# Kernel optimization log

Measured on AMD Instinct MI355X. Metric: run time of the kernel, lower is better.

The kernel has to match this reference:

```python
import jax, jax.numpy as jnp
import numpy as np

N = 50000      # nodes
E = 800000     # edges (avg degree 16)
F = 128        # num_features
H = 64         # nhid
S = 3          # num_scatter


def setup_inputs() -> dict:
    key = jax.random.key(0)
    ks = jax.random.split(key, 10)
    x = jax.random.normal(ks[0], (N, F), dtype=jnp.float32)
    scatter_edge_index = jax.random.randint(ks[1], (2, E), 0, N, dtype=jnp.int32)
    scatter_edge_attr = jax.random.normal(ks[2], (E,), dtype=jnp.float32)
    s = 0.05
    lin_W = jax.random.normal(ks[3], (F, H), dtype=jnp.float32) * s
    lin_b = jnp.zeros((H,), dtype=jnp.float32)
    # per-scatter-block 2-layer MLP applied after edge aggregation (layer=2)
    W1 = jax.random.normal(ks[4], (S, H, H), dtype=jnp.float32) * s
    b1 = jnp.zeros((S, H), dtype=jnp.float32)
    W2 = jax.random.normal(ks[5], (S, H, H), dtype=jnp.float32) * s
    b2 = jnp.zeros((S, H), dtype=jnp.float32)
    return {
        'x': x,
        'scatter_edge_index': scatter_edge_index,
        'scatter_edge_attr': scatter_edge_attr,
        'lin_W': lin_W, 'lin_b': lin_b,
        'W1': W1, 'b1': b1, 'W2': W2, 'b2': b2,
    }


def reference(x, scatter_edge_index, scatter_edge_attr, lin_W, lin_b, W1, b1, W2, b2):
    src = scatter_edge_index[0]
    dst = scatter_edge_index[1]
    attr = scatter_edge_attr[:, None]  # [E,1]

    def conv(h, i):
        # gather -> edge-weight -> scatter-add (message passing), then 2-layer MLP
        m = jax.ops.segment_sum(h[src] * attr, dst, num_segments=N)  # [N,H]
        t = jax.nn.relu(m @ W1[i] + b1[i])
        return t @ W2[i] + b2[i]

    h = x @ lin_W + lin_b  # lin_in (dropout is identity at eval)
    outs, scats = [], []
    for i in range(S):
        h = h + conv(h, i)          # residual accumulation
        outs.append(h)
        scats.append(conv(h, i))    # second conv on updated hidden_rep
    return (jnp.stack(scats), jnp.stack(outs))  # ([S,N,H], [S,N,H])
```

## Files before the change

### kernel.cpp

```cpp
#include <hip/hip_runtime.h>

#define NN 50000
#define NE 800000
#define FIN 128
#define HD 64
#define SL 3
#define GBM 782
#define NBIN 196
#define BSH 8

typedef __attribute__((ext_vector_type(8))) short bf16x8;
typedef __attribute__((ext_vector_type(4))) float f32x4;
#define MFMA(A, B, C) __builtin_amdgcn_mfma_f32_16x16x32_bf16(A, B, C, 0, 0, 0)


__device__ __forceinline__ unsigned int bfr(float x) {
    unsigned int u = __float_as_uint(x);
    return (u + 0x7fffu + ((u >> 16) & 1u)) >> 16;
}
__device__ __forceinline__ unsigned int bf2(float lo, float hi) {
    return bfr(lo) | (bfr(hi) << 16);
}


__global__ __launch_bounds__(256) void binhist_k(const int* __restrict__ dst,
                                                 int* __restrict__ bincnt) {
    __shared__ int h[256];
    int t = threadIdx.x;
    h[t] = 0;
    __syncthreads();
    int base = blockIdx.x * 4096;
    for (int i = t; i < 4096; i += 256) {
        int e = base + i;
        if (e < NE) atomicAdd(&h[dst[e] >> BSH], 1);
    }
    __syncthreads();
    if (t < NBIN && h[t]) atomicAdd(&bincnt[t], h[t]);
}

__global__ __launch_bounds__(256) void binscan_k(const int* __restrict__ bincnt,
                                                 int* __restrict__ binoff,
                                                 int* __restrict__ gbcur,
                                                 int* __restrict__ off) {
    __shared__ int sh[256];
    int t = threadIdx.x;
    int v = (t < NBIN) ? bincnt[t] : 0;
    sh[t] = v;
    __syncthreads();
    for (int d = 1; d < 256; d <<= 1) {
        int u = (t >= d) ? sh[t - d] : 0;
        __syncthreads();
        sh[t] += u;
        __syncthreads();
    }
    if (t < NBIN) {
        int ex = sh[t] - v;
        binoff[t] = ex;
        gbcur[t] = ex;
    }
    if (t == 255) {
        binoff[NBIN] = sh[255];
        off[NN] = sh[255];
    }
}

__global__ __launch_bounds__(256) void binpass_k(const int* __restrict__ src,
                                                 const int* __restrict__ dst,
                                                 const float* __restrict__ attr,
                                                 int* __restrict__ gbcur,
                                                 int2* __restrict__ tedge) {
    __shared__ int cnt_lds[256], runbase[256], lcur[256];
    int t = threadIdx.x;
    cnt_lds[t] = 0;
    lcur[t] = 0;
    __syncthreads();
    int base = blockIdx.x * 4096;
    for (int i = t; i < 4096; i += 256) {
        int e = base + i;
        if (e < NE) atomicAdd(&cnt_lds[dst[e] >> BSH], 1);
    }
    __syncthreads();
    if (t < NBIN && cnt_lds[t]) runbase[t] = atomicAdd(&gbcur[t], cnt_lds[t]);
    __syncthreads();
    for (int i = t; i < 4096; i += 256) {
        int e = base + i;
        if (e < NE) {
            int d = dst[e];
            int b = d >> BSH;
            int r = atomicAdd(&lcur[b], 1);
            tedge[runbase[b] + r] =
                make_int2(src[e] | ((d & 255) << 16), __float_as_int(attr[e]));
        }
    }
}

__global__ __launch_bounds__(256) void sortbin2_k(const int* __restrict__ binoff,
                                                  const int2* __restrict__ tedge,
                                                  int2* __restrict__ cedge,
                                                  int* __restrict__ off) {
    __shared__ int cnt[256], lofs[256], lcur[256];
    int b = blockIdx.x, t = threadIdx.x;
    int s = binoff[b], e = binoff[b + 1];
    cnt[t] = 0;
    __syncthreads();
    for (int i = s + t; i < e; i += 256)
        atomicAdd(&cnt[((unsigned)tedge[i].x >> 16) & 255], 1);
    __syncthreads();
    int v = cnt[t];
    lofs[t] = v;
    __syncthreads();
    for (int d = 1; d < 256; d <<= 1) {
        int u = (t >= d) ? lofs[t - d] : 0;
        __syncthreads();
        lofs[t] += u;
        __syncthreads();
    }
    int ex = lofs[t] - v;
    int node = (b << BSH) + t;
    if (node < NN) off[node] = s + ex;
    lcur[t] = ex;
    __syncthreads();
    for (int i = s + t; i < e; i += 256) {
        int2 ed = tedge[i];
        int dl = ((unsigned)ed.x >> 16) & 255;
        int p = s + atomicAdd(&lcur[dl], 1);
        cedge[p] = make_int2(ed.x & 0xffff, ed.y);
    }
}


__global__ __launch_bounds__(256) void wprep_k(const float* __restrict__ W1,
                                               const float* __restrict__ W2,
                                               const float* __restrict__ linW,
                                               short* __restrict__ prep) {
    int i = blockIdx.x * 256 + threadIdx.x;
    if (i < 24576) {
        int mat = i >> 12;
        int o = i & 4095;
        int j = o & 7, l = (o >> 3) & 63, s = (o >> 9) & 1, t = o >> 10;
        int k = 32 * s + 8 * (l >> 4) + j;
        int n = 16 * t + (l & 15);
        const float* Wsrc = (mat & 1) ? W2 : W1;
        prep[i] = (short)bfr(Wsrc[(mat >> 1) * 4096 + k * 64 + n]);
    } else if (i < 32768) {
        int o = i - 24576;
        int j = o & 7, l = (o >> 3) & 63, s = (o >> 9) & 3, t = o >> 11;
        int k = 32 * s + 8 * (l >> 4) + j;
        int n = 16 * t + (l & 15);
        prep[i] = (short)bfr(linW[k * 64 + n]);
    }
}


__global__ __launch_bounds__(256) void scatter_k(const uint4* __restrict__ hb4,
                                                 const int* __restrict__ off,
                                                 const int2* __restrict__ cedge,
                                                 uint4* __restrict__ mb4) {
    int w    = (blockIdx.x * blockDim.x + threadIdx.x) >> 6;
    int lane = threadIdx.x & 63;
    if (w >= NN) return;
    int g = lane >> 3;
    int f = lane & 7;
    int s = off[w], e = off[w + 1];
    float a0 = 0.f, a1 = 0.f, a2 = 0.f, a3 = 0.f;
    float a4 = 0.f, a5 = 0.f, a6 = 0.f, a7 = 0.f;
    for (int i = s + g; i < e; i += 8) {
        int2 ed = cedge[i];
        uint4 hv = hb4[(size_t)ed.x * 8 + f];
        float a = __int_as_float(ed.y);
        a0 += a * __uint_as_float(hv.x << 16);
        a1 += a * __uint_as_float(hv.x & 0xffff0000u);
        a2 += a * __uint_as_float(hv.y << 16);
        a3 += a * __uint_as_float(hv.y & 0xffff0000u);
        a4 += a * __uint_as_float(hv.z << 16);
        a5 += a * __uint_as_float(hv.z & 0xffff0000u);
        a6 += a * __uint_as_float(hv.w << 16);
        a7 += a * __uint_as_float(hv.w & 0xffff0000u);
    }
#pragma unroll
    for (int msk = 8; msk <= 32; msk <<= 1) {
        a0 += __shfl_xor(a0, msk);
        a1 += __shfl_xor(a1, msk);
        a2 += __shfl_xor(a2, msk);
        a3 += __shfl_xor(a3, msk);
        a4 += __shfl_xor(a4, msk);
        a5 += __shfl_xor(a5, msk);
        a6 += __shfl_xor(a6, msk);
        a7 += __shfl_xor(a7, msk);
    }
    if (g == 0) {
        uint4 o;
        o.x = bf2(a0, a1);
        o.y = bf2(a2, a3);
        o.z = bf2(a4, a5);
        o.w = bf2(a6, a7);
        mb4[(size_t)w * 8 + f] = o;
    }
}


__device__ __forceinline__ void conv_core(bf16x8 a0, bf16x8 a1,
                                          const bf16x8* __restrict__ w1f,
                                          const float* __restrict__ b1,
                                          const bf16x8* __restrict__ w2f,
                                          short* tw, int c, int q, int l,
                                          f32x4 oc[4]) {
    f32x4 acc[4];
#pragma unroll
    for (int t = 0; t < 4; t++) acc[t] = (f32x4){0.f, 0.f, 0.f, 0.f};
#pragma unroll
    for (int t = 0; t < 4; t++) {
        acc[t] = MFMA(a0, w1f[(t * 2 + 0) * 64 + l], acc[t]);
        acc[t] = MFMA(a1, w1f[(t * 2 + 1) * 64 + l], acc[t]);
    }
#pragma unroll
    for (int t = 0; t < 4; t++) {
        float bb = b1[16 * t + c];
#pragma unroll
        for (int rg = 0; rg < 4; rg++) {
            float v = fmaxf(acc[t][rg] + bb, 0.f);
            tw[(4 * q + rg) * 72 + 16 * t + c] = (short)bfr(v);
        }
    }
    __syncthreads();
    bf16x8 ta0 = *(const bf16x8*)&tw[c * 72 + 8 * q];
    bf16x8 ta1 = *(const bf16x8*)&tw[c * 72 + 32 + 8 * q];
#pragma unroll
    for (int t = 0; t < 4; t++) oc[t] = (f32x4){0.f, 0.f, 0.f, 0.f};
#pragma unroll
    for (int t = 0; t < 4; t++) {
        oc[t] = MFMA(ta0, w2f[(t * 2 + 0) * 64 + l], oc[t]);
        oc[t] = MFMA(ta1, w2f[(t * 2 + 1) * 64 + l], oc[t]);
    }
}


template <bool ADD, bool WB>
__global__ __launch_bounds__(256) void convm_k(const unsigned int* __restrict__ mb,
                                               const short* __restrict__ w1p,
                                               const float* __restrict__ b1,
                                               const short* __restrict__ w2p,
                                               const float* __restrict__ b2,
                                               const float* __restrict__ hprev,
                                               float* __restrict__ out,
                                               unsigned int* __restrict__ hb) {
    __shared__ short tls[4][16 * 72];
    int wv = threadIdx.x >> 6, l = threadIdx.x & 63;
    int c = l & 15, q = l >> 4;
    int rbase = blockIdx.x * 64 + wv * 16;

    int ar = rbase + c;
    bool aok = ar < NN;
    uint4 v0 = make_uint4(0, 0, 0, 0), v1 = v0;
    if (aok) {
        const uint4* mp = (const uint4*)(mb + (size_t)ar * 32);
        v0 = mp[q];
        v1 = mp[4 + q];
    }
    bf16x8 a0 = *(bf16x8*)&v0, a1 = *(bf16x8*)&v1;

    f32x4 oc[4];
    conv_core(a0, a1, (const bf16x8*)w1p, b1, (const bf16x8*)w2p, tls[wv], c, q, l, oc);

#pragma unroll
    for (int t = 0; t < 4; t++) {
        float bb = b2[16 * t + c];
#pragma unroll
        for (int rg = 0; rg < 4; rg++) {
            int row = rbase + 4 * q + rg;
            if (row < NN) {
                float v = oc[t][rg] + bb;
                if constexpr (ADD) v += hprev[(size_t)row * 64 + 16 * t + c];
                out[(size_t)row * 64 + 16 * t + c] = v;
                if constexpr (WB) {
                    float o = __shfl_xor(v, 1);
                    if ((c & 1) == 0)
                        hb[(size_t)row * 32 + 8 * t + (c >> 1)] = bf2(v, o);
                }
            }
        }
    }
}


__global__ __launch_bounds__(256) void conv2_k(const unsigned int* __restrict__ mb,
                                               const short* __restrict__ wa1,
                                               const float* __restrict__ ba1,
                                               const short* __restrict__ wa2,
                                               const float* __restrict__ ba2,
                                               const short* __restrict__ wb1,
                                               const float* __restrict__ bb1,
                                               const short* __restrict__ wb2,
                                               const float* __restrict__ bb2,
                                               const float* __restrict__ hprev,
                                               float* __restrict__ outa,
                                               float* __restrict__ outb,
                                               unsigned int* __restrict__ hb) {
    __shared__ short tls[4][16 * 72];
    int wv = threadIdx.x >> 6, l = threadIdx.x & 63;
    int c = l & 15, q = l >> 4;
    int rbase = blockIdx.x * 64 + wv * 16;

    int ar = rbase + c;
    bool aok = ar < NN;
    uint4 v0 = make_uint4(0, 0, 0, 0), v1 = v0;
    if (aok) {
        const uint4* mp = (const uint4*)(mb + (size_t)ar * 32);
        v0 = mp[q];
        v1 = mp[4 + q];
    }
    bf16x8 a0 = *(bf16x8*)&v0, a1 = *(bf16x8*)&v1;

    f32x4 oc[4];
    conv_core(a0, a1, (const bf16x8*)wa1, ba1, (const bf16x8*)wa2, tls[wv], c, q, l, oc);
#pragma unroll
    for (int t = 0; t < 4; t++) {
        float bb = ba2[16 * t + c];
#pragma unroll
        for (int rg = 0; rg < 4; rg++) {
            int row = rbase + 4 * q + rg;
            if (row < NN)
                outa[(size_t)row * 64 + 16 * t + c] = oc[t][rg] + bb;
        }
    }
    __syncthreads();

    conv_core(a0, a1, (const bf16x8*)wb1, bb1, (const bf16x8*)wb2, tls[wv], c, q, l, oc);
#pragma unroll
    for (int t = 0; t < 4; t++) {
        float bb = bb2[16 * t + c];
#pragma unroll
        for (int rg = 0; rg < 4; rg++) {
            int row = rbase + 4 * q + rg;
            if (row < NN) {
                float v = oc[t][rg] + bb + hprev[(size_t)row * 64 + 16 * t + c];
                outb[(size_t)row * 64 + 16 * t + c] = v;
                float o = __shfl_xor(v, 1);
                if ((c & 1) == 0)
                    hb[(size_t)row * 32 + 8 * t + (c >> 1)] = bf2(v, o);
            }
        }
    }
}


__global__ __launch_bounds__(256) void linm_k(const float* __restrict__ x,
                                              const short* __restrict__ wp,
                                              const float* __restrict__ b,
                                              float* __restrict__ h0,
                                              unsigned int* __restrict__ hb) {
    int wv = threadIdx.x >> 6, l = threadIdx.x & 63;
    int c = l & 15, q = l >> 4;
    int rbase = blockIdx.x * 64 + wv * 16;
    int ar = rbase + c;
    bool aok = ar < NN;

    bf16x8 af[4];
#pragma unroll
    for (int s = 0; s < 4; s++) {
        float4 p0 = make_float4(0, 0, 0, 0), p1 = p0;
        if (aok) {
            const float4* xp = (const float4*)(x + (size_t)ar * FIN + 32 * s + 8 * q);
            p0 = xp[0];
            p1 = xp[1];
        }
        bf16x8 t;
        t[0] = (short)bfr(p0.x); t[1] = (short)bfr(p0.y);
        t[2] = (short)bfr(p0.z); t[3] = (short)bfr(p0.w);
        t[4] = (short)bfr(p1.x); t[5] = (short)bfr(p1.y);
        t[6] = (short)bfr(p1.z); t[7] = (short)bfr(p1.w);
        af[s] = t;
    }

    const bf16x8* wf = (const bf16x8*)wp;
    f32x4 acc[4];
#pragma unroll
    for (int t = 0; t < 4; t++) acc[t] = (f32x4){0.f, 0.f, 0.f, 0.f};
#pragma unroll
    for (int t = 0; t < 4; t++)
#pragma unroll
        for (int s = 0; s < 4; s++)
            acc[t] = MFMA(af[s], wf[(t * 4 + s) * 64 + l], acc[t]);

#pragma unroll
    for (int t = 0; t < 4; t++) {
        float bb = b[16 * t + c];
#pragma unroll
        for (int rg = 0; rg < 4; rg++) {
            int row = rbase + 4 * q + rg;
            if (row < NN) {
                float v = acc[t][rg] + bb;
                h0[(size_t)row * 64 + 16 * t + c] = v;
                float o = __shfl_xor(v, 1);
                if ((c & 1) == 0)
                    hb[(size_t)row * 32 + 8 * t + (c >> 1)] = bf2(v, o);
            }
        }
    }
}


extern "C" void kernel_launch(void* const* d_in, const int* in_sizes, int n_in,
                              void* d_out, int out_size, void* d_ws, size_t ws_size,
                              hipStream_t stream) {
    (void)in_sizes; (void)n_in; (void)out_size; (void)ws_size;

    const float* x    = (const float*)d_in[0];
    const int*   ei   = (const int*)d_in[1];
    const float* attr = (const float*)d_in[2];
    const float* linW = (const float*)d_in[3];
    const float* linb = (const float*)d_in[4];
    const float* W1   = (const float*)d_in[5];
    const float* b1   = (const float*)d_in[6];
    const float* W2   = (const float*)d_in[7];
    const float* b2   = (const float*)d_in[8];
    float* out = (float*)d_out;

    float*        h0     = (float*)d_ws;
    unsigned int* mb     = (unsigned int*)(h0 + (size_t)NN * HD);
    unsigned int* hb     = mb + (size_t)NN * 32;
    int2*         cedge  = (int2*)(hb + (size_t)NN * 32);
    short*        prep   = (short*)(cedge + NE);
    int*          off    = (int*)(prep + 32768);
    int*          bincnt = off + NN + 1;
    int*          binoff = bincnt + 256;
    int*          gbcur  = binoff + 257;
    int2*         tedge  = (int2*)h0;

    const int* src = ei;
    const int* dst = ei + NE;

    float* scats = out;
    float* outs  = out + (size_t)SL * NN * HD;

    const size_t NH = (size_t)NN * HD;
    const int WB_ = (NN * 64) / 256;

    const short* w1p0 = prep;
    const short* w2p0 = prep + 4096;
    const short* linp = prep + 24576;

    hipMemsetAsync(bincnt, 0, 256 * sizeof(int), stream);
    binhist_k<<<196, 256, 0, stream>>>(dst, bincnt);
    binscan_k<<<1, 256, 0, stream>>>(bincnt, binoff, gbcur, off);
    binpass_k<<<196, 256, 0, stream>>>(src, dst, attr, gbcur, tedge);
    sortbin2_k<<<NBIN, 256, 0, stream>>>(binoff, tedge, cedge, off);
    wprep_k<<<128, 256, 0, stream>>>(W1, W2, linW, prep);

    linm_k<<<GBM, 256, 0, stream>>>(x, linp, linb, h0, hb);

    scatter_k<<<WB_, 256, 0, stream>>>((const uint4*)hb, off, cedge, (uint4*)mb);
    convm_k<true, true><<<GBM, 256, 0, stream>>>(mb, w1p0, b1, w2p0, b2, h0, outs, hb);

    scatter_k<<<WB_, 256, 0, stream>>>((const uint4*)hb, off, cedge, (uint4*)mb);
    conv2_k<<<GBM, 256, 0, stream>>>(mb, w1p0, b1, w2p0, b2,
                                     w1p0 + 8192, b1 + 64, w2p0 + 8192, b2 + 64,
                                     outs, scats, outs + NH, hb);

    scatter_k<<<WB_, 256, 0, stream>>>((const uint4*)hb, off, cedge, (uint4*)mb);
    conv2_k<<<GBM, 256, 0, stream>>>(mb, w1p0 + 8192, b1 + 64, w2p0 + 8192, b2 + 64,
                                     w1p0 + 16384, b1 + 128, w2p0 + 16384, b2 + 128,
                                     outs + NH, scats + NH, outs + 2 * NH, hb);

    scatter_k<<<WB_, 256, 0, stream>>>((const uint4*)hb, off, cedge, (uint4*)mb);
    convm_k<false, false><<<GBM, 256, 0, stream>>>(mb, w1p0 + 16384, b1 + 128,
                                                   w2p0 + 16384, b2 + 128,
                                                   nullptr, scats + 2 * NH, nullptr);
}
```

Before: 219.5 us.

## Replace histogram pre-pass with fixed-capacity bins during edge binning

```diff
diff --git a/kernel.cpp b/kernel.cpp
--- a/kernel.cpp
+++ b/kernel.cpp
@@ -8,6 +8,7 @@
 #define GBM 782
 #define NBIN 196
 #define BSH 8
+#define CAP 8064
 
 typedef __attribute__((ext_vector_type(8))) short bf16x8;
 typedef __attribute__((ext_vector_type(4))) float f32x4;
@@ -23,51 +24,14 @@
 }
 
 
-__global__ __launch_bounds__(256) void binhist_k(const int* __restrict__ dst,
-                                                 int* __restrict__ bincnt) {
-    __shared__ int h[256];
-    int t = threadIdx.x;
-    h[t] = 0;
-    __syncthreads();
-    int base = blockIdx.x * 4096;
-    for (int i = t; i < 4096; i += 256) {
-        int e = base + i;
-        if (e < NE) atomicAdd(&h[dst[e] >> BSH], 1);
-    }
-    __syncthreads();
-    if (t < NBIN && h[t]) atomicAdd(&bincnt[t], h[t]);
-}
-
-__global__ __launch_bounds__(256) void binscan_k(const int* __restrict__ bincnt,
-                                                 int* __restrict__ binoff,
-                                                 int* __restrict__ gbcur,
-                                                 int* __restrict__ off) {
-    __shared__ int sh[256];
-    int t = threadIdx.x;
-    int v = (t < NBIN) ? bincnt[t] : 0;
-    sh[t] = v;
-    __syncthreads();
-    for (int d = 1; d < 256; d <<= 1) {
-        int u = (t >= d) ? sh[t - d] : 0;
-        __syncthreads();
-        sh[t] += u;
-        __syncthreads();
-    }
-    if (t < NBIN) {
-        int ex = sh[t] - v;
-        binoff[t] = ex;
-        gbcur[t] = ex;
-    }
-    if (t == 255) {
-        binoff[NBIN] = sh[255];
-        off[NN] = sh[255];
-    }
+__global__ void zero_k(int* __restrict__ g) {
+    if (threadIdx.x < NBIN) g[threadIdx.x] = 0;
 }
 
 __global__ __launch_bounds__(256) void binpass_k(const int* __restrict__ src,
                                                  const int* __restrict__ dst,
                                                  const float* __restrict__ attr,
-                                                 int* __restrict__ gbcur,
+                                                 int* __restrict__ gcur,
                                                  int2* __restrict__ tedge) {
     __shared__ int cnt_lds[256], runbase[256], lcur[256];
     int t = threadIdx.x;
@@ -80,7 +44,7 @@
         if (e < NE) atomicAdd(&cnt_lds[dst[e] >> BSH], 1);
     }
     __syncthreads();
-    if (t < NBIN && cnt_lds[t]) runbase[t] = atomicAdd(&gbcur[t], cnt_lds[t]);
+    if (t < NBIN && cnt_lds[t]) runbase[t] = atomicAdd(&gcur[t], cnt_lds[t]);
     __syncthreads();
     for (int i = t; i < 4096; i += 256) {
         int e = base + i;
@@ -88,9 +52,30 @@
             int d = dst[e];
             int b = d >> BSH;
             int r = atomicAdd(&lcur[b], 1);
-            tedge[runbase[b] + r] =
+            tedge[(size_t)b * CAP + runbase[b] + r] =
                 make_int2(src[e] | ((d & 255) << 16), __float_as_int(attr[e]));
         }
+    }
+}
+
+__global__ __launch_bounds__(256) void binscan_k(const int* __restrict__ gcur,
+                                                 int* __restrict__ binoff,
+                                                 int* __restrict__ off) {
+    __shared__ int sh[256];
+    int t = threadIdx.x;
+    int v = (t < NBIN) ? gcur[t] : 0;
+    sh[t] = v;
+    __syncthreads();
+    for (int d = 1; d < 256; d <<= 1) {
+        int u = (t >= d) ? sh[t - d] : 0;
+        __syncthreads();
+        sh[t] += u;
+        __syncthreads();
+    }
+    if (t < NBIN) binoff[t] = sh[t] - v;
+    if (t == 255) {
+        binoff[NBIN] = sh[255];
+        off[NN] = sh[255];
     }
 }
 
@@ -100,11 +85,13 @@
                                                   int* __restrict__ off) {
     __shared__ int cnt[256], lofs[256], lcur[256];
     int b = blockIdx.x, t = threadIdx.x;
-    int s = binoff[b], e = binoff[b + 1];
+    int s = binoff[b];
+    int n_in_bin = binoff[b + 1] - s;
+    const int2* tb = tedge + (size_t)b * CAP;
     cnt[t] = 0;
     __syncthreads();
-    for (int i = s + t; i < e; i += 256)
-        atomicAdd(&cnt[((unsigned)tedge[i].x >> 16) & 255], 1);
+    for (int i = t; i < n_in_bin; i += 256)
+        atomicAdd(&cnt[((unsigned)tb[i].x >> 16) & 255], 1);
     __syncthreads();
     int v = cnt[t];
     lofs[t] = v;
@@ -120,8 +107,8 @@
     if (node < NN) off[node] = s + ex;
     lcur[t] = ex;
     __syncthreads();
-    for (int i = s + t; i < e; i += 256) {
-        int2 ed = tedge[i];
+    for (int i = t; i < n_in_bin; i += 256) {
+        int2 ed = tb[i];
         int dl = ((unsigned)ed.x >> 16) & 255;
         int p = s + atomicAdd(&lcur[dl], 1);
         cedge[p] = make_int2(ed.x & 0xffff, ed.y);
@@ -422,9 +409,8 @@
     int2*         cedge  = (int2*)(hb + (size_t)NN * 32);
     short*        prep   = (short*)(cedge + NE);
     int*          off    = (int*)(prep + 32768);
-    int*          bincnt = off + NN + 1;
-    int*          binoff = bincnt + 256;
-    int*          gbcur  = binoff + 257;
+    int*          gcur   = off + NN + 1;
+    int*          binoff = gcur + 256;
     int2*         tedge  = (int2*)h0;
 
     const int* src = ei;
@@ -440,10 +426,9 @@
     const short* w2p0 = prep + 4096;
     const short* linp = prep + 24576;
 
-    hipMemsetAsync(bincnt, 0, 256 * sizeof(int), stream);
-    binhist_k<<<196, 256, 0, stream>>>(dst, bincnt);
-    binscan_k<<<1, 256, 0, stream>>>(bincnt, binoff, gbcur, off);
-    binpass_k<<<196, 256, 0, stream>>>(src, dst, attr, gbcur, tedge);
+    zero_k<<<1, 256, 0, stream>>>(gcur);
+    binpass_k<<<196, 256, 0, stream>>>(src, dst, attr, gcur, tedge);
+    binscan_k<<<1, 256, 0, stream>>>(gcur, binoff, off);
     sortbin2_k<<<NBIN, 256, 0, stream>>>(binoff, tedge, cedge, off);
     wprep_k<<<128, 256, 0, stream>>>(W1, W2, linW, prep);
 
```

Result: faster. 209.2 us (-4.7%).
